# Kernel tuning notes

Hardware: AMD Instinct MI355X
Metric: run time of the kernel (lower is better)

## Reference

```python
import jax, jax.numpy as jnp
import numpy as np

N = 10000        # nodes
E = 320000       # edges (avg degree 32)
K = 3            # TAGConv default hops
D_IN, D_H, D_OUT = 256, 128, 64


def setup_inputs() -> dict:
    key = jax.random.key(0)
    ks = jax.random.split(key, 12)
    def w(k, shape):
        # xavier-uniform-ish init
        fan_in, fan_out = shape[-2], shape[-1]
        lim = float(np.sqrt(6.0 / (fan_in + fan_out)))
        return jax.random.uniform(k, shape, jnp.float32, -lim, lim)
    return {
        "x": jax.random.normal(ks[0], (N, D_IN), dtype=jnp.float32),
        "edge_index": jax.random.randint(ks[1], (2, E), 0, N, dtype=jnp.int32),
        "W1": w(ks[2], (K + 1, D_IN, D_H)),  "b1": jnp.zeros((D_H,), jnp.float32),
        "W2": w(ks[3], (K + 1, D_H, D_H)),   "b2": jnp.zeros((D_H,), jnp.float32),
        "W3": w(ks[4], (K + 1, D_H, D_OUT)), "b3": jnp.zeros((D_OUT,), jnp.float32),
        "Wf": w(ks[5], (D_OUT, D_OUT)),      "bf": jnp.zeros((D_OUT,), jnp.float32),
        "Wd": w(ks[6], (D_OUT, D_OUT)),
    }


def _gcn_norm(src, dst, n_nodes):
    # TAGConv's gcn_norm without self-loops: D^-1/2 A D^-1/2 edge weights
    deg = jax.ops.segment_sum(jnp.ones(src.shape, jnp.float32), dst,
                              num_segments=n_nodes)
    dis = jnp.where(deg > 0, jax.lax.rsqrt(jnp.maximum(deg, 1.0)), 0.0)
    return dis[src] * dis[dst]  # [E]


def _tagconv(x, src, dst, norm, W, b):
    # out = sum_{k=0..K} (A_hat^k x) @ W[k] + b
    out = x @ W[0]
    h = x
    for k in range(1, W.shape[0]):
        # message = norm_e * h[src_e], aggregated at dst
        h = jax.ops.segment_sum(norm[:, None] * h[src], dst,
                                num_segments=x.shape[0])
        out = out + h @ W[k]
    return out + b


def reference(x, edge_index, W1, b1, W2, b2, W3, b3, Wf, bf, Wd):
    src, dst = edge_index[0], edge_index[1]
    norm = _gcn_norm(src, dst, x.shape[0])
    h = jax.nn.relu(_tagconv(x, src, dst, norm, W1, b1))
    h = jax.nn.relu(_tagconv(h, src, dst, norm, W2, b2))
    h = jax.nn.relu(_tagconv(h, src, dst, norm, W3, b3))
    z = h @ Wf + bf                     # [N, D_OUT]
    adj = (z @ Wd) @ z.T                # [N, N] bilinear decode
    return adj
```

## Files before the change

kernel.cpp:

```cpp
#include <hip/hip_runtime.h>
#include <hip/hip_bf16.h>
#include <cstdint>
#include <cstddef>


typedef __attribute__((ext_vector_type(8)))  short short8;
typedef __attribute__((ext_vector_type(4)))  float f32x4;
typedef __attribute__((ext_vector_type(16))) float f32x16;

static __device__ __forceinline__ ushort f2bf(float f) {
    __hip_bfloat16 h = __float2bfloat16(f);
    return *reinterpret_cast<const ushort*>(&h);
}
static __device__ __forceinline__ float bf2f(ushort u) {
    union { uint i; float f; } v; v.i = ((uint)u) << 16; return v.f;
}


static __device__ __forceinline__ void prep_w_elem(const float* W, ushort* Wp,
                                                   int DIN, int DOUT, int i) {
    int hp  = i / (DIN * DOUT);
    int rem = i - hp * DIN * DOUT;
    int d   = rem / DOUT;
    int o   = rem - d * DOUT;
    Wp[(size_t)(hp * DOUT + o) * DIN + d] = f2bf(W[i]);
}
static __device__ __forceinline__ void prep_wt_elem(const float* W, ushort* Wt,
                                                    int K, int C, int i) {
    int k = i / C, c = i - k * C;
    Wt[(size_t)c * K + k] = f2bf(W[i]);
}

__global__ void setup_kernel(const int* __restrict__ dst, int* __restrict__ counts, int E,
                             const float* __restrict__ x, ushort* __restrict__ xb, int nx4,
                             const float* __restrict__ W1, ushort* __restrict__ Wp1,
                             const float* __restrict__ W2, ushort* __restrict__ Wp2,
                             const float* __restrict__ W3, ushort* __restrict__ Wp3,
                             const float* __restrict__ Wf, ushort* __restrict__ Wfb,
                             const float* __restrict__ Wd, ushort* __restrict__ Wdb) {
    const int n1 = 4 * 256 * 128, n2 = 4 * 128 * 128, n3 = 4 * 128 * 64, nf = 64 * 64;
    int i = blockIdx.x * blockDim.x + threadIdx.x;
    if (i < E) atomicAdd(&counts[dst[i]], 1);
    if (i < nx4) {
        float4 v = ((const float4*)x)[i];
        ushort4 o;
        o.x = f2bf(v.x); o.y = f2bf(v.y); o.z = f2bf(v.z); o.w = f2bf(v.w);
        ((ushort4*)xb)[i] = o;
        return;
    }
    int j = i - nx4;
    if (j < n1) { prep_w_elem(W1, Wp1, 256, 128, j); return; }
    j -= n1;
    if (j < n2) { prep_w_elem(W2, Wp2, 128, 128, j); return; }
    j -= n2;
    if (j < n3) { prep_w_elem(W3, Wp3, 128, 64, j); return; }
    j -= n3;
    if (j < nf) { prep_wt_elem(Wf, Wfb, 64, 64, j); return; }
    j -= nf;
    if (j < nf) { prep_wt_elem(Wd, Wdb, 64, 64, j); return; }
}

__global__ void scan_kernel(const int* __restrict__ counts, int* __restrict__ rowstart,
                            float* __restrict__ dis, int n) {
    __shared__ int sums[1024];
    int t = threadIdx.x;
    int chunk = (n + 1023) / 1024;
    int base = t * chunk;
    int s = 0;
    for (int i = 0; i < chunk; ++i) {
        int idx = base + i;
        if (idx < n) s += counts[idx];
    }
    sums[t] = s;
    __syncthreads();
    for (int off = 1; off < 1024; off <<= 1) {
        int v = (t >= off) ? sums[t - off] : 0;
        __syncthreads();
        sums[t] += v;
        __syncthreads();
    }
    int run = sums[t] - s;
    for (int i = 0; i < chunk; ++i) {
        int idx = base + i;
        if (idx < n) {
            rowstart[idx] = run;
            int c = counts[idx];
            dis[idx] = (c > 0) ? rsqrtf((float)c) : 0.f;
            run += c;
        }
    }
    if (t == 1023) rowstart[n] = sums[1023];
}

__global__ void csr_fill_kernel(const int* __restrict__ src, const int* __restrict__ dst,
                                const float* __restrict__ dis, const int* __restrict__ rowstart,
                                int* __restrict__ cursor, int2* __restrict__ csr2, int E) {
    int e = blockIdx.x * blockDim.x + threadIdx.x;
    if (e < E) {
        int d = dst[e];
        int s = src[e];
        int pos = rowstart[d] + atomicAdd(&cursor[d], 1);
        csr2[pos] = make_int2(s, __float_as_int(dis[s] * dis[d]));
    }
}

template <int DIN, int DOUT>
__global__ __launch_bounds__(256) void proj_gemm_kernel(
        const ushort* __restrict__ A, const ushort* __restrict__ Wp,
        const float* __restrict__ bias, ushort* __restrict__ y, int M) {
    constexpr int NJ = DOUT / 16;
    int tid = threadIdx.x, wave = tid >> 6, lane = tid & 63;
    int lr = lane & 15, lk = lane >> 4;
    int r0 = blockIdx.x * 32;
    int ra0 = min(r0 + lr, M - 1);
    int ra1 = min(r0 + 16 + lr, M - 1);

    f32x4 acc[2][NJ];
    #pragma unroll
    for (int mi = 0; mi < 2; ++mi)
        #pragma unroll
        for (int nj = 0; nj < NJ; ++nj)
            acc[mi][nj] = (f32x4){0.f, 0.f, 0.f, 0.f};

    const ushort* a0p = A + (size_t)ra0 * DIN + lk * 8;
    const ushort* a1p = A + (size_t)ra1 * DIN + lk * 8;
    #pragma unroll
    for (int kc = 0; kc < DIN; kc += 32) {
        short8 a0 = *(const short8*)(a0p + kc);
        short8 a1 = *(const short8*)(a1p + kc);
        #pragma unroll
        for (int nj = 0; nj < NJ; ++nj) {
            short8 b = *(const short8*)(Wp + (size_t)(wave * DOUT + nj * 16 + lr) * DIN
                                        + kc + lk * 8);
            acc[0][nj] = __builtin_amdgcn_mfma_f32_16x16x32_bf16(a0, b, acc[0][nj], 0, 0, 0);
            acc[1][nj] = __builtin_amdgcn_mfma_f32_16x16x32_bf16(a1, b, acc[1][nj], 0, 0, 0);
        }
    }

    ushort* yw = y + (size_t)wave * M * DOUT;
    #pragma unroll
    for (int nj = 0; nj < NJ; ++nj) {
        int c = nj * 16 + lr;
        float bv = (wave == 0) ? bias[c] : 0.f;
        #pragma unroll
        for (int mi = 0; mi < 2; ++mi) {
            int rbase = r0 + mi * 16 + lk * 4;
            #pragma unroll
            for (int r = 0; r < 4; ++r) {
                int row = rbase + r;
                if (row < M)
                    yw[(size_t)row * DOUT + c] = f2bf(acc[mi][nj][r] + bv);
            }
        }
    }
}

template <int D, bool RELU>
__global__ __launch_bounds__(512) void agg6_kernel(
        const ushort* __restrict__ h, const ushort* __restrict__ yk,
        const int* __restrict__ rowstart, const int2* __restrict__ csr2,
        ushort* __restrict__ out, int Nn) {
    constexpr int LPE = D / 8;
    constexpr int EPI = 64 / LPE;
    int wave = threadIdx.x >> 6, lane = threadIdx.x & 63;
    int n = blockIdx.x * 8 + wave;
    if (n >= Nn) return;
    int sub = lane / LPE;
    int ll  = lane % LPE;
    int beg = rowstart[n], end = rowstart[n + 1];

    float acc[8];
    #pragma unroll
    for (int v = 0; v < 8; ++v) acc[v] = 0.f;

    for (int j0 = beg; j0 < end; j0 += 64) {
        int take = end - j0;
        if (take > 64) take = 64;
        int2 ed = make_int2(0, 0);
        if (lane < take) ed = csr2[j0 + lane];
        int   s = ed.x;
        float w = __int_as_float(ed.y);
        int tt = (take + EPI - 1) & ~(EPI - 1);

        float wc = __shfl(w, sub);
        int   sc = __shfl(s, sub);
        short8 hv = *(const short8*)(h + (size_t)sc * D + ll * 8);
        for (int i = EPI; i < tt; i += EPI) {
            float wn = __shfl(w, i + sub);
            int   sn = __shfl(s, i + sub);
            short8 hn = *(const short8*)(h + (size_t)sn * D + ll * 8);
            #pragma unroll
            for (int v = 0; v < 8; ++v)
                acc[v] = fmaf(wc, bf2f((ushort)hv[v]), acc[v]);
            wc = wn; hv = hn;
        }
        #pragma unroll
        for (int v = 0; v < 8; ++v)
            acc[v] = fmaf(wc, bf2f((ushort)hv[v]), acc[v]);
    }

    #pragma unroll
    for (int off = LPE; off < 64; off <<= 1) {
        #pragma unroll
        for (int v = 0; v < 8; ++v) acc[v] += __shfl_xor(acc[v], off);
    }

    if (sub == 0) {
        short8 yv = *(const short8*)(yk + (size_t)n * D + ll * 8);
        short8 o;
        #pragma unroll
        for (int v = 0; v < 8; ++v) {
            float val = acc[v] + bf2f((ushort)yv[v]);
            if (RELU) val = fmaxf(val, 0.f);
            o[v] = (short)f2bf(val);
        }
        *(short8*)(out + (size_t)n * D + ll * 8) = o;
    }
}

__global__ __launch_bounds__(256) void lin64_dual_kernel(
        const ushort* __restrict__ A, const ushort* __restrict__ Wfb,
        const float* __restrict__ bias, const ushort* __restrict__ Wdb,
        ushort* __restrict__ zz, ushort* __restrict__ zw, int M) {
    __shared__ ushort zl[4][32][72];
    int tid = threadIdx.x, wave = tid >> 6, lane = tid & 63;
    int lr = lane & 15, lk = lane >> 4;
    int r0 = blockIdx.x * 128 + wave * 32;
    int ra0 = min(r0 + lr, M - 1);
    int ra1 = min(r0 + 16 + lr, M - 1);

    short8 a[2][2], b[4][2];
    #pragma unroll
    for (int kc = 0; kc < 2; ++kc) {
        a[0][kc] = *(const short8*)(A + (size_t)ra0 * 64 + kc * 32 + lk * 8);
        a[1][kc] = *(const short8*)(A + (size_t)ra1 * 64 + kc * 32 + lk * 8);
        #pragma unroll
        for (int nj = 0; nj < 4; ++nj)
            b[nj][kc] = *(const short8*)(Wfb + (size_t)(nj * 16 + lr) * 64 + kc * 32 + lk * 8);
    }
    f32x4 acc1[2][4];
    #pragma unroll
    for (int mi = 0; mi < 2; ++mi)
        #pragma unroll
        for (int nj = 0; nj < 4; ++nj) {
            acc1[mi][nj] = (f32x4){0.f, 0.f, 0.f, 0.f};
            acc1[mi][nj] = __builtin_amdgcn_mfma_f32_16x16x32_bf16(a[mi][0], b[nj][0], acc1[mi][nj], 0, 0, 0);
            acc1[mi][nj] = __builtin_amdgcn_mfma_f32_16x16x32_bf16(a[mi][1], b[nj][1], acc1[mi][nj], 0, 0, 0);
        }

    #pragma unroll
    for (int nj = 0; nj < 4; ++nj) {
        int c = nj * 16 + lr;
        float bv = bias[c];
        #pragma unroll
        for (int mi = 0; mi < 2; ++mi) {
            int rloc = mi * 16 + lk * 4;
            #pragma unroll
            for (int r = 0; r < 4; ++r) {
                ushort u = f2bf(acc1[mi][nj][r] + bv);
                zl[wave][rloc + r][c] = u;
                int row = r0 + rloc + r;
                if (row < M) zz[(size_t)row * 64 + c] = u;
            }
        }
    }
    __syncthreads();

    short8 a2[2][2], b2[4][2];
    #pragma unroll
    for (int kc = 0; kc < 2; ++kc) {
        a2[0][kc] = *(const short8*)&zl[wave][lr][kc * 32 + lk * 8];
        a2[1][kc] = *(const short8*)&zl[wave][16 + lr][kc * 32 + lk * 8];
        #pragma unroll
        for (int nj = 0; nj < 4; ++nj)
            b2[nj][kc] = *(const short8*)(Wdb + (size_t)(nj * 16 + lr) * 64 + kc * 32 + lk * 8);
    }
    f32x4 acc2[2][4];
    #pragma unroll
    for (int mi = 0; mi < 2; ++mi)
        #pragma unroll
        for (int nj = 0; nj < 4; ++nj) {
            acc2[mi][nj] = (f32x4){0.f, 0.f, 0.f, 0.f};
            acc2[mi][nj] = __builtin_amdgcn_mfma_f32_16x16x32_bf16(a2[mi][0], b2[nj][0], acc2[mi][nj], 0, 0, 0);
            acc2[mi][nj] = __builtin_amdgcn_mfma_f32_16x16x32_bf16(a2[mi][1], b2[nj][1], acc2[mi][nj], 0, 0, 0);
        }
    #pragma unroll
    for (int nj = 0; nj < 4; ++nj) {
        int c = nj * 16 + lr;
        #pragma unroll
        for (int mi = 0; mi < 2; ++mi) {
            int rbase = r0 + mi * 16 + lk * 4;
            #pragma unroll
            for (int r = 0; r < 4; ++r) {
                int row = rbase + r;
                if (row < M) zw[(size_t)row * 64 + c] = f2bf(acc2[mi][nj][r]);
            }
        }
    }
}

__global__ __launch_bounds__(256) void decode32_kernel(
        const ushort* __restrict__ ZW, const ushort* __restrict__ Z,
        float* __restrict__ out, int Nn) {
    int tid = threadIdx.x, wave = tid >> 6, lane = tid & 63;
    int wr = wave >> 1, wc = wave & 1;
    int row0 = blockIdx.y * 128 + wr * 64;
    int col0 = blockIdx.x * 128 + wc * 64;
    int lr = lane & 31, hi = lane >> 5;

    short8 a[2][4], b[2][4];
    #pragma unroll
    for (int mi = 0; mi < 2; ++mi) {
        int ra = min(row0 + mi * 32 + lr, Nn - 1);
        int rb = min(col0 + mi * 32 + lr, Nn - 1);
        const ushort* pa = ZW + (size_t)ra * 64 + hi * 8;
        const ushort* pb = Z  + (size_t)rb * 64 + hi * 8;
        #pragma unroll
        for (int kc = 0; kc < 4; ++kc) {
            a[mi][kc] = *(const short8*)(pa + kc * 16);
            b[mi][kc] = *(const short8*)(pb + kc * 16);
        }
    }

    f32x16 acc[2][2];
    #pragma unroll
    for (int mi = 0; mi < 2; ++mi)
        #pragma unroll
        for (int nj = 0; nj < 2; ++nj) {
            f32x16 c;
            #pragma unroll
            for (int q = 0; q < 16; ++q) c[q] = 0.f;
            #pragma unroll
            for (int kc = 0; kc < 4; ++kc)
                c = __builtin_amdgcn_mfma_f32_32x32x16_bf16(a[mi][kc], b[nj][kc], c, 0, 0, 0);
            acc[mi][nj] = c;
        }

    bool full = (row0 + 64 <= Nn) && (col0 + 64 <= Nn);
    #pragma unroll
    for (int mi = 0; mi < 2; ++mi)
        #pragma unroll
        for (int nj = 0; nj < 2; ++nj) {
            int cb = col0 + nj * 32 + lr;
            #pragma unroll
            for (int reg = 0; reg < 16; ++reg) {
                int row = row0 + mi * 32 + (reg & 3) + 8 * (reg >> 2) + 4 * hi;
                if (full) {
                    __builtin_nontemporal_store(acc[mi][nj][reg], &out[(size_t)row * Nn + cb]);
                } else {
                    if (row < Nn && cb < Nn)
                        __builtin_nontemporal_store(acc[mi][nj][reg], &out[(size_t)row * Nn + cb]);
                }
            }
        }
}


extern "C" void kernel_launch(void* const* d_in, const int* in_sizes, int n_in,
                              void* d_out, int out_size, void* d_ws, size_t ws_size,
                              hipStream_t stream) {
    const float* x  = (const float*)d_in[0];
    const int*   ei = (const int*)d_in[1];
    const float* W1 = (const float*)d_in[2];
    const float* b1 = (const float*)d_in[3];
    const float* W2 = (const float*)d_in[4];
    const float* b2 = (const float*)d_in[5];
    const float* W3 = (const float*)d_in[6];
    const float* b3 = (const float*)d_in[7];
    const float* Wf = (const float*)d_in[8];
    const float* bf = (const float*)d_in[9];
    const float* Wd = (const float*)d_in[10];

    const int Nn = in_sizes[0] / 256;
    const int E  = in_sizes[1] / 2;
    const int* src = ei;
    const int* dst = ei + E;

    char* p = (char*)d_ws;
    auto alloc = [&](size_t bytes) -> char* {
        char* r = p;
        p += (bytes + 255) & ~(size_t)255;
        return r;
    };
    size_t nslot = ((size_t)Nn * 4 + 255) & ~(size_t)255;
    int*    counts   = (int*)alloc((size_t)Nn * 4);
    int*    cursor   = (int*)alloc((size_t)Nn * 4);
    int*    rowstart = (int*)alloc((size_t)(Nn + 1) * 4);
    float*  dis      = (float*)alloc((size_t)Nn * 4);
    int2*   csr2     = (int2*)alloc((size_t)E * 8);
    ushort* xb       = (ushort*)alloc((size_t)Nn * 256 * 2);
    ushort* yb       = (ushort*)alloc((size_t)4 * Nn * 128 * 2);
    ushort* t1       = (ushort*)alloc((size_t)Nn * 128 * 2);
    ushort* t2       = (ushort*)alloc((size_t)Nn * 128 * 2);
    ushort* out1b    = (ushort*)alloc((size_t)Nn * 128 * 2);
    ushort* out2b    = (ushort*)alloc((size_t)Nn * 128 * 2);
    ushort* out3b    = (ushort*)alloc((size_t)Nn * 64 * 2);
    ushort* zzb      = (ushort*)alloc((size_t)Nn * 64 * 2);
    ushort* zwb      = (ushort*)alloc((size_t)Nn * 64 * 2);
    ushort* Wp1      = (ushort*)alloc((size_t)512 * 256 * 2);
    ushort* Wp2      = (ushort*)alloc((size_t)512 * 128 * 2);
    ushort* Wp3      = (ushort*)alloc((size_t)256 * 128 * 2);
    ushort* Wfb      = (ushort*)alloc((size_t)64 * 64 * 2);
    ushort* Wdb      = (ushort*)alloc((size_t)64 * 64 * 2);

    hipMemsetAsync(counts, 0, nslot + (size_t)Nn * 4, stream);

    int nx4 = Nn * 256 / 4;
    int nprep = nx4 + 4 * 256 * 128 + 4 * 128 * 128 + 4 * 128 * 64 + 64 * 64 + 64 * 64;
    int nsetup = nprep > E ? nprep : E;
    setup_kernel<<<(nsetup + 255) / 256, 256, 0, stream>>>(
        dst, counts, E, x, xb, nx4,
        W1, Wp1, W2, Wp2, W3, Wp3, Wf, Wfb, Wd, Wdb);

    scan_kernel<<<1, 1024, 0, stream>>>(counts, rowstart, dis, Nn);

    int eb = (E + 255) / 256;
    csr_fill_kernel<<<eb, 256, 0, stream>>>(src, dst, dis, rowstart, cursor, csr2, E);

    int ab = (Nn + 7) / 8;
    int gb = (Nn + 31) / 32;
    size_t Y128 = (size_t)Nn * 128;
    size_t Y64  = (size_t)Nn * 64;

    proj_gemm_kernel<256, 128><<<gb, 256, 0, stream>>>(xb, Wp1, b1, yb, Nn);
    agg6_kernel<128, false><<<ab, 512, 0, stream>>>(yb + 3 * Y128, yb + 2 * Y128,
                                                    rowstart, csr2, t1, Nn);
    agg6_kernel<128, false><<<ab, 512, 0, stream>>>(t1, yb + 1 * Y128,
                                                    rowstart, csr2, t2, Nn);
    agg6_kernel<128, true ><<<ab, 512, 0, stream>>>(t2, yb,
                                                    rowstart, csr2, out1b, Nn);

    proj_gemm_kernel<128, 128><<<gb, 256, 0, stream>>>(out1b, Wp2, b2, yb, Nn);
    agg6_kernel<128, false><<<ab, 512, 0, stream>>>(yb + 3 * Y128, yb + 2 * Y128,
                                                    rowstart, csr2, t1, Nn);
    agg6_kernel<128, false><<<ab, 512, 0, stream>>>(t1, yb + 1 * Y128,
                                                    rowstart, csr2, t2, Nn);
    agg6_kernel<128, true ><<<ab, 512, 0, stream>>>(t2, yb,
                                                    rowstart, csr2, out2b, Nn);

    proj_gemm_kernel<128, 64><<<gb, 256, 0, stream>>>(out2b, Wp3, b3, yb, Nn);
    agg6_kernel<64, false><<<ab, 512, 0, stream>>>(yb + 3 * Y64, yb + 2 * Y64,
                                                   rowstart, csr2, t1, Nn);
    agg6_kernel<64, false><<<ab, 512, 0, stream>>>(t1, yb + 1 * Y64,
                                                   rowstart, csr2, t2, Nn);
    agg6_kernel<64, true ><<<ab, 512, 0, stream>>>(t2, yb,
                                                   rowstart, csr2, out3b, Nn);

    int lb = (Nn + 127) / 128;
    lin64_dual_kernel<<<lb, 256, 0, stream>>>(out3b, Wfb, bf, Wdb, zzb, zwb, Nn);

    int db = (Nn + 127) / 128;
    decode32_kernel<<<dim3(db, db), 256, 0, stream>>>(zwb, zzb, (float*)d_out, Nn);
}
```

Baseline: 324.0 us.

## Fuse final aggregation with next projection and fold x bf16 cast into GEMM

The last aggregation hop of each TAGConv layer (with bias and ReLU) is fused with the next layer's projection GEMM, or with the final linear and decode-weight GEMMs, by staging 32 aggregated rows in shared memory before running MFMA. The first projection reads fp32 x directly and converts to bf16 in registers, so the separate x conversion pass in setup and the xb buffer go away. Each layer now gets its own projection buffer, since the fused kernel reads the previous y0 while writing the new one. This removes several kernel launches and a round trip of intermediate activations through global memory. The cost is that each fused block does its 32-node gather and then a GEMM, and in the last kernel only one wave does the MFMA work.

```diff
diff --git a/kernel.cpp b/kernel.cpp
--- a/kernel.cpp
+++ b/kernel.cpp
@@ -32,7 +32,6 @@
 }
 
 __global__ void setup_kernel(const int* __restrict__ dst, int* __restrict__ counts, int E,
-                             const float* __restrict__ x, ushort* __restrict__ xb, int nx4,
                              const float* __restrict__ W1, ushort* __restrict__ Wp1,
                              const float* __restrict__ W2, ushort* __restrict__ Wp2,
                              const float* __restrict__ W3, ushort* __restrict__ Wp3,
@@ -41,16 +40,8 @@
     const int n1 = 4 * 256 * 128, n2 = 4 * 128 * 128, n3 = 4 * 128 * 64, nf = 64 * 64;
     int i = blockIdx.x * blockDim.x + threadIdx.x;
     if (i < E) atomicAdd(&counts[dst[i]], 1);
-    if (i < nx4) {
-        float4 v = ((const float4*)x)[i];
-        ushort4 o;
-        o.x = f2bf(v.x); o.y = f2bf(v.y); o.z = f2bf(v.z); o.w = f2bf(v.w);
-        ((ushort4*)xb)[i] = o;
-        return;
-    }
-    int j = i - nx4;
-    if (j < n1) { prep_w_elem(W1, Wp1, 256, 128, j); return; }
-    j -= n1;
+    if (i < n1) { prep_w_elem(W1, Wp1, 256, 128, i); return; }
+    int j = i - n1;
     if (j < n2) { prep_w_elem(W2, Wp2, 128, 128, j); return; }
     j -= n2;
     if (j < n3) { prep_w_elem(W3, Wp3, 128, 64, j); return; }
@@ -104,75 +95,12 @@
     }
 }
 
-template <int DIN, int DOUT>
-__global__ __launch_bounds__(256) void proj_gemm_kernel(
-        const ushort* __restrict__ A, const ushort* __restrict__ Wp,
-        const float* __restrict__ bias, ushort* __restrict__ y, int M) {
-    constexpr int NJ = DOUT / 16;
-    int tid = threadIdx.x, wave = tid >> 6, lane = tid & 63;
-    int lr = lane & 15, lk = lane >> 4;
-    int r0 = blockIdx.x * 32;
-    int ra0 = min(r0 + lr, M - 1);
-    int ra1 = min(r0 + 16 + lr, M - 1);
-
-    f32x4 acc[2][NJ];
-    #pragma unroll
-    for (int mi = 0; mi < 2; ++mi)
-        #pragma unroll
-        for (int nj = 0; nj < NJ; ++nj)
-            acc[mi][nj] = (f32x4){0.f, 0.f, 0.f, 0.f};
-
-    const ushort* a0p = A + (size_t)ra0 * DIN + lk * 8;
-    const ushort* a1p = A + (size_t)ra1 * DIN + lk * 8;
-    #pragma unroll
-    for (int kc = 0; kc < DIN; kc += 32) {
-        short8 a0 = *(const short8*)(a0p + kc);
-        short8 a1 = *(const short8*)(a1p + kc);
-        #pragma unroll
-        for (int nj = 0; nj < NJ; ++nj) {
-            short8 b = *(const short8*)(Wp + (size_t)(wave * DOUT + nj * 16 + lr) * DIN
-                                        + kc + lk * 8);
-            acc[0][nj] = __builtin_amdgcn_mfma_f32_16x16x32_bf16(a0, b, acc[0][nj], 0, 0, 0);
-            acc[1][nj] = __builtin_amdgcn_mfma_f32_16x16x32_bf16(a1, b, acc[1][nj], 0, 0, 0);
-        }
-    }
-
-    ushort* yw = y + (size_t)wave * M * DOUT;
-    #pragma unroll
-    for (int nj = 0; nj < NJ; ++nj) {
-        int c = nj * 16 + lr;
-        float bv = (wave == 0) ? bias[c] : 0.f;
-        #pragma unroll
-        for (int mi = 0; mi < 2; ++mi) {
-            int rbase = r0 + mi * 16 + lk * 4;
-            #pragma unroll
-            for (int r = 0; r < 4; ++r) {
-                int row = rbase + r;
-                if (row < M)
-                    yw[(size_t)row * DOUT + c] = f2bf(acc[mi][nj][r] + bv);
-            }
-        }
-    }
-}
-
-template <int D, bool RELU>
-__global__ __launch_bounds__(512) void agg6_kernel(
-        const ushort* __restrict__ h, const ushort* __restrict__ yk,
-        const int* __restrict__ rowstart, const int2* __restrict__ csr2,
-        ushort* __restrict__ out, int Nn) {
+template <int D>
+static __device__ __forceinline__ void agg_gather(
+        const ushort* __restrict__ h, const int2* __restrict__ csr2,
+        int beg, int end, int lane, int sub, int ll, float acc[8]) {
     constexpr int LPE = D / 8;
     constexpr int EPI = 64 / LPE;
-    int wave = threadIdx.x >> 6, lane = threadIdx.x & 63;
-    int n = blockIdx.x * 8 + wave;
-    if (n >= Nn) return;
-    int sub = lane / LPE;
-    int ll  = lane % LPE;
-    int beg = rowstart[n], end = rowstart[n + 1];
-
-    float acc[8];
-    #pragma unroll
-    for (int v = 0; v < 8; ++v) acc[v] = 0.f;
-
     for (int j0 = beg; j0 < end; j0 += 64) {
         int take = end - j0;
         if (take > 64) take = 64;
@@ -198,6 +126,24 @@
         for (int v = 0; v < 8; ++v)
             acc[v] = fmaf(wc, bf2f((ushort)hv[v]), acc[v]);
     }
+}
+
+template <int D, bool RELU>
+__global__ __launch_bounds__(512) void agg6_kernel(
+        const ushort* __restrict__ h, const ushort* __restrict__ yk,
+        const int* __restrict__ rowstart, const int2* __restrict__ csr2,
+        ushort* __restrict__ out, int Nn) {
+    constexpr int LPE = D / 8;
+    int wave = threadIdx.x >> 6, lane = threadIdx.x & 63;
+    int n = blockIdx.x * 8 + wave;
+    if (n >= Nn) return;
+    int sub = lane / LPE;
+    int ll  = lane % LPE;
+
+    float acc[8];
+    #pragma unroll
+    for (int v = 0; v < 8; ++v) acc[v] = 0.f;
+    agg_gather<D>(h, csr2, rowstart[n], rowstart[n + 1], lane, sub, ll, acc);
 
     #pragma unroll
     for (int off = LPE; off < 64; off <<= 1) {
@@ -218,82 +164,240 @@
     }
 }
 
-__global__ __launch_bounds__(256) void lin64_dual_kernel(
-        const ushort* __restrict__ A, const ushort* __restrict__ Wfb,
-        const float* __restrict__ bias, const ushort* __restrict__ Wdb,
-        ushort* __restrict__ zz, ushort* __restrict__ zw, int M) {
-    __shared__ ushort zl[4][32][72];
+template <int DIN, int DOUT>
+__global__ __launch_bounds__(512) void fused_agg_proj_kernel(
+        const ushort* __restrict__ h, const ushort* __restrict__ y0,
+        const int* __restrict__ rowstart, const int2* __restrict__ csr2,
+        const ushort* __restrict__ Wp, const float* __restrict__ bias,
+        ushort* __restrict__ y, int Nn) {
+    __shared__ ushort sh[32][DIN + 8];
+    constexpr int LPE = DIN / 8;
+    int wave = threadIdx.x >> 6, lane = threadIdx.x & 63;
+    int nb0 = blockIdx.x * 32;
+    int sub = lane / LPE, ll = lane % LPE;
+
+    for (int c = 0; c < 4; ++c) {
+        int nl = wave * 4 + c;
+        int nc = min(nb0 + nl, Nn - 1);
+        float acc[8];
+        #pragma unroll
+        for (int v = 0; v < 8; ++v) acc[v] = 0.f;
+        agg_gather<DIN>(h, csr2, rowstart[nc], rowstart[nc + 1], lane, sub, ll, acc);
+        #pragma unroll
+        for (int off = LPE; off < 64; off <<= 1) {
+            #pragma unroll
+            for (int v = 0; v < 8; ++v) acc[v] += __shfl_xor(acc[v], off);
+        }
+        if (sub == 0) {
+            short8 yv = *(const short8*)(y0 + (size_t)nc * DIN + ll * 8);
+            short8 o;
+            #pragma unroll
+            for (int v = 0; v < 8; ++v)
+                o[v] = (short)f2bf(fmaxf(acc[v] + bf2f((ushort)yv[v]), 0.f));
+            *(short8*)&sh[nl][ll * 8] = o;
+        }
+    }
+    __syncthreads();
+
+    constexpr int NJ = DOUT / 16;
+    int hp = wave & 3, half = wave >> 2;
+    int lr = lane & 15, lk = lane >> 4;
+
+    f32x4 pacc[NJ];
+    #pragma unroll
+    for (int nj = 0; nj < NJ; ++nj) pacc[nj] = (f32x4){0.f, 0.f, 0.f, 0.f};
+
+    #pragma unroll
+    for (int kc = 0; kc < DIN; kc += 32) {
+        short8 a = *(const short8*)&sh[half * 16 + lr][kc + lk * 8];
+        #pragma unroll
+        for (int nj = 0; nj < NJ; ++nj) {
+            short8 b = *(const short8*)(Wp + (size_t)(hp * DOUT + nj * 16 + lr) * DIN
+                                        + kc + lk * 8);
+            pacc[nj] = __builtin_amdgcn_mfma_f32_16x16x32_bf16(a, b, pacc[nj], 0, 0, 0);
+        }
+    }
+
+    ushort* yw = y + (size_t)hp * Nn * DOUT;
+    #pragma unroll
+    for (int nj = 0; nj < NJ; ++nj) {
+        int cc = nj * 16 + lr;
+        float bv = (hp == 0) ? bias[cc] : 0.f;
+        int rbase = nb0 + half * 16 + lk * 4;
+        #pragma unroll
+        for (int r = 0; r < 4; ++r) {
+            int row = rbase + r;
+            if (row < Nn)
+                yw[(size_t)row * DOUT + cc] = f2bf(pacc[nj][r] + bv);
+        }
+    }
+}
+
+__global__ __launch_bounds__(512) void fused_agg_lin_kernel(
+        const ushort* __restrict__ h, const ushort* __restrict__ y0,
+        const int* __restrict__ rowstart, const int2* __restrict__ csr2,
+        const ushort* __restrict__ Wfb, const float* __restrict__ bias,
+        const ushort* __restrict__ Wdb,
+        ushort* __restrict__ zz, ushort* __restrict__ zw, int Nn) {
+    __shared__ ushort sh[32][72];
+    __shared__ ushort sh2[32][72];
+    constexpr int DIN = 64, LPE = 8;
+    int wave = threadIdx.x >> 6, lane = threadIdx.x & 63;
+    int nb0 = blockIdx.x * 32;
+    int sub = lane / LPE, ll = lane % LPE;
+
+    for (int c = 0; c < 4; ++c) {
+        int nl = wave * 4 + c;
+        int nc = min(nb0 + nl, Nn - 1);
+        float acc[8];
+        #pragma unroll
+        for (int v = 0; v < 8; ++v) acc[v] = 0.f;
+        agg_gather<DIN>(h, csr2, rowstart[nc], rowstart[nc + 1], lane, sub, ll, acc);
+        #pragma unroll
+        for (int off = LPE; off < 64; off <<= 1) {
+            #pragma unroll
+            for (int v = 0; v < 8; ++v) acc[v] += __shfl_xor(acc[v], off);
+        }
+        if (sub == 0) {
+            short8 yv = *(const short8*)(y0 + (size_t)nc * DIN + ll * 8);
+            short8 o;
+            #pragma unroll
+            for (int v = 0; v < 8; ++v)
+                o[v] = (short)f2bf(fmaxf(acc[v] + bf2f((ushort)yv[v]), 0.f));
+            *(short8*)&sh[nl][ll * 8] = o;
+        }
+    }
+    __syncthreads();
+
+    int lr = lane & 15, lk = lane >> 4;
+    if (wave == 0) {
+        short8 a[2][2], b[4][2];
+        #pragma unroll
+        for (int kc = 0; kc < 2; ++kc) {
+            a[0][kc] = *(const short8*)&sh[lr][kc * 32 + lk * 8];
+            a[1][kc] = *(const short8*)&sh[16 + lr][kc * 32 + lk * 8];
+            #pragma unroll
+            for (int nj = 0; nj < 4; ++nj)
+                b[nj][kc] = *(const short8*)(Wfb + (size_t)(nj * 16 + lr) * 64 + kc * 32 + lk * 8);
+        }
+        f32x4 acc1[2][4];
+        #pragma unroll
+        for (int mi = 0; mi < 2; ++mi)
+            #pragma unroll
+            for (int nj = 0; nj < 4; ++nj) {
+                acc1[mi][nj] = (f32x4){0.f, 0.f, 0.f, 0.f};
+                acc1[mi][nj] = __builtin_amdgcn_mfma_f32_16x16x32_bf16(a[mi][0], b[nj][0], acc1[mi][nj], 0, 0, 0);
+                acc1[mi][nj] = __builtin_amdgcn_mfma_f32_16x16x32_bf16(a[mi][1], b[nj][1], acc1[mi][nj], 0, 0, 0);
+            }
+        #pragma unroll
+        for (int nj = 0; nj < 4; ++nj) {
+            int cc = nj * 16 + lr;
+            float bv = bias[cc];
+            #pragma unroll
+            for (int mi = 0; mi < 2; ++mi) {
+                int rloc = mi * 16 + lk * 4;
+                #pragma unroll
+                for (int r = 0; r < 4; ++r) {
+                    ushort u = f2bf(acc1[mi][nj][r] + bv);
+                    sh2[rloc + r][cc] = u;
+                    int row = nb0 + rloc + r;
+                    if (row < Nn) zz[(size_t)row * 64 + cc] = u;
+                }
+            }
+        }
+    }
+    __syncthreads();
+    if (wave == 0) {
+        short8 a2[2][2], b2[4][2];
+        #pragma unroll
+        for (int kc = 0; kc < 2; ++kc) {
+            a2[0][kc] = *(const short8*)&sh2[lr][kc * 32 + lk * 8];
+            a2[1][kc] = *(const short8*)&sh2[16 + lr][kc * 32 + lk * 8];
+            #pragma unroll
+            for (int nj = 0; nj < 4; ++nj)
+                b2[nj][kc] = *(const short8*)(Wdb + (size_t)(nj * 16 + lr) * 64 + kc * 32 + lk * 8);
+        }
+        f32x4 acc2[2][4];
+        #pragma unroll
+        for (int mi = 0; mi < 2; ++mi)
+            #pragma unroll
+            for (int nj = 0; nj < 4; ++nj) {
+                acc2[mi][nj] = (f32x4){0.f, 0.f, 0.f, 0.f};
+                acc2[mi][nj] = __builtin_amdgcn_mfma_f32_16x16x32_bf16(a2[mi][0], b2[nj][0], acc2[mi][nj], 0, 0, 0);
+                acc2[mi][nj] = __builtin_amdgcn_mfma_f32_16x16x32_bf16(a2[mi][1], b2[nj][1], acc2[mi][nj], 0, 0, 0);
+            }
+        #pragma unroll
+        for (int nj = 0; nj < 4; ++nj) {
+            int cc = nj * 16 + lr;
+            #pragma unroll
+            for (int mi = 0; mi < 2; ++mi) {
+                int rbase = nb0 + mi * 16 + lk * 4;
+                #pragma unroll
+                for (int r = 0; r < 4; ++r) {
+                    int row = rbase + r;
+                    if (row < Nn) zw[(size_t)row * 64 + cc] = f2bf(acc2[mi][nj][r]);
+                }
+            }
+        }
+    }
+}
+
+__global__ __launch_bounds__(256) void proj_gemm_x_kernel(
+        const float* __restrict__ A, const ushort* __restrict__ Wp,
+        const float* __restrict__ bias, ushort* __restrict__ y, int M) {
+    constexpr int DIN = 256, DOUT = 128, NJ = 8;
     int tid = threadIdx.x, wave = tid >> 6, lane = tid & 63;
     int lr = lane & 15, lk = lane >> 4;
-    int r0 = blockIdx.x * 128 + wave * 32;
+    int r0 = blockIdx.x * 32;
     int ra0 = min(r0 + lr, M - 1);
     int ra1 = min(r0 + 16 + lr, M - 1);
 
-    short8 a[2][2], b[4][2];
-    #pragma unroll
-    for (int kc = 0; kc < 2; ++kc) {
-        a[0][kc] = *(const short8*)(A + (size_t)ra0 * 64 + kc * 32 + lk * 8);
-        a[1][kc] = *(const short8*)(A + (size_t)ra1 * 64 + kc * 32 + lk * 8);
-        #pragma unroll
-        for (int nj = 0; nj < 4; ++nj)
-            b[nj][kc] = *(const short8*)(Wfb + (size_t)(nj * 16 + lr) * 64 + kc * 32 + lk * 8);
-    }
-    f32x4 acc1[2][4];
+    f32x4 acc[2][NJ];
     #pragma unroll
     for (int mi = 0; mi < 2; ++mi)
         #pragma unroll
-        for (int nj = 0; nj < 4; ++nj) {
-            acc1[mi][nj] = (f32x4){0.f, 0.f, 0.f, 0.f};
-            acc1[mi][nj] = __builtin_amdgcn_mfma_f32_16x16x32_bf16(a[mi][0], b[nj][0], acc1[mi][nj], 0, 0, 0);
-            acc1[mi][nj] = __builtin_amdgcn_mfma_f32_16x16x32_bf16(a[mi][1], b[nj][1], acc1[mi][nj], 0, 0, 0);
-        }
-
-    #pragma unroll
-    for (int nj = 0; nj < 4; ++nj) {
+        for (int nj = 0; nj < NJ; ++nj)
+            acc[mi][nj] = (f32x4){0.f, 0.f, 0.f, 0.f};
+
+    const float* a0p = A + (size_t)ra0 * DIN + lk * 8;
+    const float* a1p = A + (size_t)ra1 * DIN + lk * 8;
+    #pragma unroll
+    for (int kc = 0; kc < DIN; kc += 32) {
+        float4 f00 = *(const float4*)(a0p + kc);
+        float4 f01 = *(const float4*)(a0p + kc + 4);
+        float4 f10 = *(const float4*)(a1p + kc);
+        float4 f11 = *(const float4*)(a1p + kc + 4);
+        short8 a0, a1;
+        a0[0] = (short)f2bf(f00.x); a0[1] = (short)f2bf(f00.y);
+        a0[2] = (short)f2bf(f00.z); a0[3] = (short)f2bf(f00.w);
+        a0[4] = (short)f2bf(f01.x); a0[5] = (short)f2bf(f01.y);
+        a0[6] = (short)f2bf(f01.z); a0[7] = (short)f2bf(f01.w);
+        a1[0] = (short)f2bf(f10.x); a1[1] = (short)f2bf(f10.y);
+        a1[2] = (short)f2bf(f10.z); a1[3] = (short)f2bf(f10.w);
+        a1[4] = (short)f2bf(f11.x); a1[5] = (short)f2bf(f11.y);
+        a1[6] = (short)f2bf(f11.z); a1[7] = (short)f2bf(f11.w);
+        #pragma unroll
+        for (int nj = 0; nj < NJ; ++nj) {
+            short8 b = *(const short8*)(Wp + (size_t)(wave * DOUT + nj * 16 + lr) * DIN
+                                        + kc + lk * 8);
+            acc[0][nj] = __builtin_amdgcn_mfma_f32_16x16x32_bf16(a0, b, acc[0][nj], 0, 0, 0);
+            acc[1][nj] = __builtin_amdgcn_mfma_f32_16x16x32_bf16(a1, b, acc[1][nj], 0, 0, 0);
+        }
+    }
+
+    ushort* yw = y + (size_t)wave * M * DOUT;
+    #pragma unroll
+    for (int nj = 0; nj < NJ; ++nj) {
         int c = nj * 16 + lr;
-        float bv = bias[c];
-        #pragma unroll
-        for (int mi = 0; mi < 2; ++mi) {
-            int rloc = mi * 16 + lk * 4;
-            #pragma unroll
-            for (int r = 0; r < 4; ++r) {
-                ushort u = f2bf(acc1[mi][nj][r] + bv);
-                zl[wave][rloc + r][c] = u;
-                int row = r0 + rloc + r;
-                if (row < M) zz[(size_t)row * 64 + c] = u;
-            }
-        }
-    }
-    __syncthreads();
-
-    short8 a2[2][2], b2[4][2];
-    #pragma unroll
-    for (int kc = 0; kc < 2; ++kc) {
-        a2[0][kc] = *(const short8*)&zl[wave][lr][kc * 32 + lk * 8];
-        a2[1][kc] = *(const short8*)&zl[wave][16 + lr][kc * 32 + lk * 8];
-        #pragma unroll
-        for (int nj = 0; nj < 4; ++nj)
-            b2[nj][kc] = *(const short8*)(Wdb + (size_t)(nj * 16 + lr) * 64 + kc * 32 + lk * 8);
-    }
-    f32x4 acc2[2][4];
-    #pragma unroll
-    for (int mi = 0; mi < 2; ++mi)
-        #pragma unroll
-        for (int nj = 0; nj < 4; ++nj) {
-            acc2[mi][nj] = (f32x4){0.f, 0.f, 0.f, 0.f};
-            acc2[mi][nj] = __builtin_amdgcn_mfma_f32_16x16x32_bf16(a2[mi][0], b2[nj][0], acc2[mi][nj], 0, 0, 0);
-            acc2[mi][nj] = __builtin_amdgcn_mfma_f32_16x16x32_bf16(a2[mi][1], b2[nj][1], acc2[mi][nj], 0, 0, 0);
-        }
-    #pragma unroll
-    for (int nj = 0; nj < 4; ++nj) {
-        int c = nj * 16 + lr;
+        float bv = (wave == 0) ? bias[c] : 0.f;
         #pragma unroll
         for (int mi = 0; mi < 2; ++mi) {
             int rbase = r0 + mi * 16 + lk * 4;
             #pragma unroll
             for (int r = 0; r < 4; ++r) {
                 int row = rbase + r;
-                if (row < M) zw[(size_t)row * 64 + c] = f2bf(acc2[mi][nj][r]);
+                if (row < M)
+                    yw[(size_t)row * DOUT + c] = f2bf(acc[mi][nj][r] + bv);
             }
         }
     }
@@ -388,13 +492,11 @@
     int*    rowstart = (int*)alloc((size_t)(Nn + 1) * 4);
     float*  dis      = (float*)alloc((size_t)Nn * 4);
     int2*   csr2     = (int2*)alloc((size_t)E * 8);
-    ushort* xb       = (ushort*)alloc((size_t)Nn * 256 * 2);
-    ushort* yb       = (ushort*)alloc((size_t)4 * Nn * 128 * 2);
+    ushort* yb1      = (ushort*)alloc((size_t)4 * Nn * 128 * 2);
+    ushort* yb2      = (ushort*)alloc((size_t)4 * Nn * 128 * 2);
+    ushort* yb3      = (ushort*)alloc((size_t)4 * Nn * 64 * 2);
     ushort* t1       = (ushort*)alloc((size_t)Nn * 128 * 2);
     ushort* t2       = (ushort*)alloc((size_t)Nn * 128 * 2);
-    ushort* out1b    = (ushort*)alloc((size_t)Nn * 128 * 2);
-    ushort* out2b    = (ushort*)alloc((size_t)Nn * 128 * 2);
-    ushort* out3b    = (ushort*)alloc((size_t)Nn * 64 * 2);
     ushort* zzb      = (ushort*)alloc((size_t)Nn * 64 * 2);
     ushort* zwb      = (ushort*)alloc((size_t)Nn * 64 * 2);
     ushort* Wp1      = (ushort*)alloc((size_t)512 * 256 * 2);
@@ -405,12 +507,10 @@
 
     hipMemsetAsync(counts, 0, nslot + (size_t)Nn * 4, stream);
 
-    int nx4 = Nn * 256 / 4;
-    int nprep = nx4 + 4 * 256 * 128 + 4 * 128 * 128 + 4 * 128 * 64 + 64 * 64 + 64 * 64;
+    int nprep = 4 * 256 * 128 + 4 * 128 * 128 + 4 * 128 * 64 + 64 * 64 + 64 * 64;
     int nsetup = nprep > E ? nprep : E;
     setup_kernel<<<(nsetup + 255) / 256, 256, 0, stream>>>(
-        dst, counts, E, x, xb, nx4,
-        W1, Wp1, W2, Wp2, W3, Wp3, Wf, Wfb, Wd, Wdb);
+        dst, counts, E, W1, Wp1, W2, Wp2, W3, Wp3, Wf, Wfb, Wd, Wdb);
 
     scan_kernel<<<1, 1024, 0, stream>>>(counts, rowstart, dis, Nn);
 
@@ -422,32 +522,27 @@
     size_t Y128 = (size_t)Nn * 128;
     size_t Y64  = (size_t)Nn * 64;
 
-    proj_gemm_kernel<256, 128><<<gb, 256, 0, stream>>>(xb, Wp1, b1, yb, Nn);
-    agg6_kernel<128, false><<<ab, 512, 0, stream>>>(yb + 3 * Y128, yb + 2 * Y128,
+    proj_gemm_x_kernel<<<gb, 256, 0, stream>>>(x, Wp1, b1, yb1, Nn);
+    agg6_kernel<128, false><<<ab, 512, 0, stream>>>(yb1 + 3 * Y128, yb1 + 2 * Y128,
                                                     rowstart, csr2, t1, Nn);
-    agg6_kernel<128, false><<<ab, 512, 0, stream>>>(t1, yb + 1 * Y128,
+    agg6_kernel<128, false><<<ab, 512, 0, stream>>>(t1, yb1 + 1 * Y128,
                                                     rowstart, csr2, t2, Nn);
-    agg6_kernel<128, true ><<<ab, 512, 0, stream>>>(t2, yb,
-                                                    rowstart, csr2, out1b, Nn);
-
-    proj_gemm_kernel<128, 128><<<gb, 256, 0, stream>>>(out1b, Wp2, b2, yb, Nn);
-    agg6_kernel<128, false><<<ab, 512, 0, stream>>>(yb + 3 * Y128, yb + 2 * Y128,
+    fused_agg_proj_kernel<128, 128><<<gb, 512, 0, stream>>>(t2, yb1, rowstart, csr2,
+                                                            Wp2, b2, yb2, Nn);
+
+    agg6_kernel<128, false><<<ab, 512, 0, stream>>>(yb2 + 3 * Y128, yb2 + 2 * Y128,
                                                     rowstart, csr2, t1, Nn);
-    agg6_kernel<128, false><<<ab, 512, 0, stream>>>(t1, yb + 1 * Y128,
+    agg6_kernel<128, false><<<ab, 512, 0, stream>>>(t1, yb2 + 1 * Y128,
                                                     rowstart, csr2, t2, Nn);
-    agg6_kernel<128, true ><<<ab, 512, 0, stream>>>(t2, yb,
-                                                    rowstart, csr2, out2b, Nn);
-
-    proj_gemm_kernel<128, 64><<<gb, 256, 0, stream>>>(out2b, Wp3, b3, yb, Nn);
-    agg6_kernel<64, false><<<ab, 512, 0, stream>>>(yb + 3 * Y64, yb + 2 * Y64,
+    fused_agg_proj_kernel<128, 64><<<gb, 512, 0, stream>>>(t2, yb2, rowstart, csr2,
+                                                           Wp3, b3, yb3, Nn);
+
+    agg6_kernel<64, false><<<ab, 512, 0, stream>>>(yb3 + 3 * Y64, yb3 + 2 * Y64,
                                                    rowstart, csr2, t1, Nn);
-    agg6_kernel<64, false><<<ab, 512, 0, stream>>>(t1, yb + 1 * Y64,
+    agg6_kernel<64, false><<<ab, 512, 0, stream>>>(t1, yb3 + 1 * Y64,
                                                    rowstart, csr2, t2, Nn);
-    agg6_kernel<64, true ><<<ab, 512, 0, stream>>>(t2, yb,
-                                                   rowstart, csr2, out3b, Nn);
-
-    int lb = (Nn + 127) / 128;
-    lin64_dual_kernel<<<lb, 256, 0, stream>>>(out3b, Wfb, bf, Wdb, zzb, zwb, Nn);
+    fused_agg_lin_kernel<<<gb, 512, 0, stream>>>(t2, yb3, rowstart, csr2,
+                                                 Wfb, bf, Wdb, zzb, zwb, Nn);
 
     int db = (Nn + 127) / 128;
     decode32_kernel<<<dim3(db, db), 256, 0, stream>>>(zwb, zzb, (float*)d_out, Nn);
```

After: 333.7 us. 3.0% more time.
